# Optimization experiments

Hardware: AMD Instinct MI355X
Metric: run time of the kernel (lower is better)

## Reference

```python
import jax, jax.numpy as jnp
import numpy as np

N_NODES = 100000
N_EDGES = 1600000
HIDDEN = 64
N_MID = 3  # num_layers=5 -> 1 first + 3 middle + 1 last


def setup_inputs() -> dict:
    key = jax.random.key(0)
    ks = jax.random.split(key, 12)
    x = jax.random.normal(ks[0], (N_NODES, 1), dtype=jnp.float32)
    edge_index = jax.random.randint(ks[1], (2, N_EDGES), 0, N_NODES, dtype=jnp.int32)
    edge_weight = jax.random.uniform(ks[2], (N_EDGES,), dtype=jnp.float32)
    s0 = 1.0  # fan_in=1
    sh = 1.0 / np.sqrt(HIDDEN)
    Wrel0 = jax.random.normal(ks[3], (HIDDEN, 1), dtype=jnp.float32) * s0
    brel0 = jax.random.normal(ks[4], (HIDDEN,), dtype=jnp.float32) * s0
    Wroot0 = jax.random.normal(ks[5], (HIDDEN, 1), dtype=jnp.float32) * s0
    Wrel_mid = jax.random.normal(ks[6], (N_MID, HIDDEN, HIDDEN), dtype=jnp.float32) * sh
    brel_mid = jax.random.normal(ks[7], (N_MID, HIDDEN), dtype=jnp.float32) * sh
    Wroot_mid = jax.random.normal(ks[8], (N_MID, HIDDEN, HIDDEN), dtype=jnp.float32) * sh
    WrelL = jax.random.normal(ks[9], (1, HIDDEN), dtype=jnp.float32) * sh
    brelL = jax.random.normal(ks[10], (1,), dtype=jnp.float32) * sh
    WrootL = jax.random.normal(ks[11], (1, HIDDEN), dtype=jnp.float32) * sh
    return {"x": x, "edge_index": edge_index, "edge_weight": edge_weight,
            "Wrel0": Wrel0, "brel0": brel0, "Wroot0": Wroot0,
            "Wrel_mid": Wrel_mid, "brel_mid": brel_mid, "Wroot_mid": Wroot_mid,
            "WrelL": WrelL, "brelL": brelL, "WrootL": WrootL}


def reference(x, edge_index, edge_weight, Wrel0, brel0, Wroot0,
              Wrel_mid, brel_mid, Wroot_mid, WrelL, brelL, WrootL):
    src = edge_index[0]
    dst = edge_index[1]
    n = x.shape[0]

    def conv(h, Wrel, brel, Wroot):
        # PyG GraphConv(aggr='add'): lin_rel(sum_j w_ij * h_j) + lin_root(h_i)
        msg = h[src] * edge_weight[:, None]          # [E, C]
        agg = jax.ops.segment_sum(msg, dst, num_segments=n)  # [N, C]
        return agg @ Wrel.T + brel + h @ Wroot.T

    # dropout omitted (deterministic reference); relu after all but last layer
    h = jax.nn.relu(conv(x, Wrel0, brel0, Wroot0))
    for i in range(Wrel_mid.shape[0]):
        h = jax.nn.relu(conv(h, Wrel_mid[i], brel_mid[i], Wroot_mid[i]))
    return conv(h, WrelL, brelL, WrootL)  # [N, 1]
```

## Files before the change

kernel.cpp:

```cpp
#include <hip/hip_runtime.h>
#include <stdint.h>


#define NN 100000
#define NE 1600000
#define HID 64
#define NBKT 391
#define CAP 8192
#define PMAX (NBKT * CAP)
#define TILE 4096
#define EPT 16
#define NTILE ((NE + TILE - 1) / TILE)

typedef __attribute__((ext_vector_type(8))) short bf16x8;
typedef __attribute__((ext_vector_type(4))) float f32x4;
typedef __attribute__((ext_vector_type(2))) unsigned int u32x2;
typedef __attribute__((ext_vector_type(4))) unsigned int u32x4;

__device__ __forceinline__ uint32_t rne_bf16(float v) {
    uint32_t u = __float_as_uint(v);
    return (u + 0x7fffu + ((u >> 16) & 1u)) >> 16;
}


__global__ __launch_bounds__(256) void k_bpart(const int* __restrict__ src,
                                               const int* __restrict__ dst,
                                               const float* __restrict__ w,
                                               int* __restrict__ bcur,
                                               int2* __restrict__ bpairs) {
    __shared__ int  hcnt[NBKT];
    __shared__ int  hoff[NBKT];
    __shared__ int  hadj[NBKT];
    __shared__ int  sc0[512];
    __shared__ int  sc1[512];
    __shared__ int2 sT[TILE];
    __shared__ int  sAdj[TILE];
    int tile0 = blockIdx.x * TILE;
    int t = threadIdx.x;
    for (int i = t; i < NBKT; i += 256) hcnt[i] = 0;
    __syncthreads();

    int   pk[EPT];
    int   bk[EPT];
    float wv[EPT];
    #pragma unroll
    for (int k = 0; k < EPT; k++) {
        int e = tile0 + t + k * 256;
        if (e < NE) {
            int d = dst[e];
            int b = d >> 8;
            pk[k] = (src[e] << 8) | (d & 255);
            wv[k] = w[e];
            bk[k] = b;
            atomicAdd(&hcnt[b], 1);
        } else {
            bk[k] = -1;
        }
    }
    __syncthreads();

    sc0[t]       = (t < NBKT) ? hcnt[t] : 0;
    sc0[t + 256] = (t + 256 < NBKT) ? hcnt[t + 256] : 0;
    __syncthreads();
    int* cur = sc0;
    int* oth = sc1;
    for (int off = 1; off < 512; off <<= 1) {
        int v0 = cur[t]       + ((t       >= off) ? cur[t - off]       : 0);
        int v1 = cur[t + 256] + ((t + 256 >= off) ? cur[t + 256 - off] : 0);
        oth[t] = v0;
        oth[t + 256] = v1;
        __syncthreads();
        int* tmp = cur; cur = oth; oth = tmp;
    }
    for (int i = t; i < NBKT; i += 256) {
        int c = hcnt[i];
        int excl = cur[i] - c;
        hoff[i] = excl;
        int gbase = c ? atomicAdd(&bcur[i], c) : 0;
        hadj[i] = gbase - excl;
        hcnt[i] = 0;
    }
    __syncthreads();

    #pragma unroll
    for (int k = 0; k < EPT; k++) {
        if (bk[k] >= 0) {
            int b = bk[k];
            int pos = hoff[b] + atomicAdd(&hcnt[b], 1);
            sT[pos] = make_int2(pk[k], __float_as_int(wv[k]));
            sAdj[pos] = hadj[b];
        }
    }
    __syncthreads();

    int n = NE - tile0; if (n > TILE) n = TILE;
    for (int j = t; j < n; j += 256)
        bpairs[sAdj[j] + j] = sT[j];
}

__global__ __launch_bounds__(256) void k_bcsr(const int* __restrict__ bcur,
                                              const int2* __restrict__ bpairs,
                                              int* __restrict__ offs,
                                              int* __restrict__ ends,
                                              uint32_t* __restrict__ pairs) {
    __shared__ int2 sE[CAP];
    __shared__ int cnt[256];
    __shared__ int scn[256];
    __shared__ int cur[256];
    int k = blockIdx.x, t = threadIdx.x;
    int base = k * CAP;
    int scnt = bcur[k] - base;
    cnt[t] = 0;
    __syncthreads();
    for (int j = t; j < scnt; j += 256) {
        int2 q = bpairs[base + j];
        sE[j] = q;
        atomicAdd(&cnt[q.x & 255], 1);
    }
    __syncthreads();
    int v = cnt[t], acc = v;
    scn[t] = v;
    __syncthreads();
    for (int off = 1; off < 256; off <<= 1) {
        int u = (t >= off) ? scn[t - off] : 0;
        __syncthreads();
        acc += u;
        scn[t] = acc;
        __syncthreads();
    }
    int excl = acc - v;
    cur[t] = excl;
    int d = (k << 8) + t;
    if (d < NN) {
        offs[d] = base + excl;
        ends[d] = base + excl + v;
    }
    __syncthreads();
    for (int j = t; j < scnt; j += 256) {
        int2 q = sE[j];
        int pos = base + atomicAdd(&cur[q.x & 255], 1);
        uint32_t wb = rne_bf16(__int_as_float(q.y)) & 0x7fffu;
        pairs[pos] = (wb << 17) | (uint32_t)(q.x >> 8);
    }
}


__global__ __launch_bounds__(256) void k_wsplit(const float* __restrict__ Wrel_mid,
                                                const float* __restrict__ Wroot_mid,
                                                uint16_t* __restrict__ WgH,
                                                uint16_t* __restrict__ WgL,
                                                uint16_t* __restrict__ WrH,
                                                uint16_t* __restrict__ WrL,
                                                int* __restrict__ bcur) {
    int i = blockIdx.x * blockDim.x + threadIdx.x;
    if (i < NBKT) bcur[i] = i * CAP;
    if (i >= 3 * 4096) return;
    float a = Wrel_mid[i];
    uint32_t ah = rne_bf16(a);
    float al = a - __uint_as_float(ah << 16);
    WgH[i] = (uint16_t)ah;
    WgL[i] = (uint16_t)rne_bf16(al);
    float b = Wroot_mid[i];
    uint32_t bh = rne_bf16(b);
    float bl = b - __uint_as_float(bh << 16);
    WrH[i] = (uint16_t)bh;
    WrL[i] = (uint16_t)rne_bf16(bl);
}


__device__ __forceinline__ void mfma_epilogue(
        int lane, int w, const uint32_t* sH,
        const uint16_t* __restrict__ WgH, const uint16_t* __restrict__ WgL,
        const uint16_t* __restrict__ WrH, const uint16_t* __restrict__ WrL,
        const float* __restrict__ brel,
        uint16_t* sG, uint16_t* sR) {
    int row = lane & 15;
    int quad = lane >> 4;
    int kb = quad * 8;
    bf16x8 ah0 = *(const bf16x8*)&sH[row * 36 + quad * 4];
    bf16x8 ah1 = *(const bf16x8*)&sH[row * 36 + 16 + quad * 4];
    int oc = w * 16 + row;
    {
        bf16x8 bh0 = *(const bf16x8*)&WgH[oc * 64 + kb];
        bf16x8 bh1 = *(const bf16x8*)&WgH[oc * 64 + 32 + kb];
        bf16x8 bl0 = *(const bf16x8*)&WgL[oc * 64 + kb];
        bf16x8 bl1 = *(const bf16x8*)&WgL[oc * 64 + 32 + kb];
        f32x4 acc = {0.f, 0.f, 0.f, 0.f};
        acc = __builtin_amdgcn_mfma_f32_16x16x32_bf16(ah0, bh0, acc, 0, 0, 0);
        acc = __builtin_amdgcn_mfma_f32_16x16x32_bf16(ah1, bh1, acc, 0, 0, 0);
        acc = __builtin_amdgcn_mfma_f32_16x16x32_bf16(ah0, bl0, acc, 0, 0, 0);
        acc = __builtin_amdgcn_mfma_f32_16x16x32_bf16(ah1, bl1, acc, 0, 0, 0);
        #pragma unroll
        for (int r = 0; r < 4; r++)
            sG[(quad * 4 + r) * 68 + oc] = (uint16_t)rne_bf16(acc[r]);
    }
    {
        bf16x8 bh0 = *(const bf16x8*)&WrH[oc * 64 + kb];
        bf16x8 bh1 = *(const bf16x8*)&WrH[oc * 64 + 32 + kb];
        bf16x8 bl0 = *(const bf16x8*)&WrL[oc * 64 + kb];
        bf16x8 bl1 = *(const bf16x8*)&WrL[oc * 64 + 32 + kb];
        float bias = brel[oc];
        f32x4 acc = {bias, bias, bias, bias};
        acc = __builtin_amdgcn_mfma_f32_16x16x32_bf16(ah0, bh0, acc, 0, 0, 0);
        acc = __builtin_amdgcn_mfma_f32_16x16x32_bf16(ah1, bh1, acc, 0, 0, 0);
        acc = __builtin_amdgcn_mfma_f32_16x16x32_bf16(ah0, bl0, acc, 0, 0, 0);
        acc = __builtin_amdgcn_mfma_f32_16x16x32_bf16(ah1, bl1, acc, 0, 0, 0);
        #pragma unroll
        for (int r = 0; r < 4; r++)
            sR[(quad * 4 + r) * 68 + oc] = (uint16_t)rne_bf16(acc[r]);
    }
}

__device__ __forceinline__ void epilogue_writeout(
        int tid, int blk16, const uint16_t* sG, const uint16_t* sR,
        uint16_t* __restrict__ Gout, uint16_t* __restrict__ Rout) {
    const uint32_t* sGd = (const uint32_t*)sG;
    const uint32_t* sRd = (const uint32_t*)sR;
    uint32_t* Gd = (uint32_t*)Gout;
    uint32_t* Rd = (uint32_t*)Rout;
    #pragma unroll
    for (int it = 0; it < 2; it++) {
        int idx = it * 256 + tid;
        int nd = idx >> 5, col = idx & 31;
        Gd[(blk16 + nd) * 32 + col] = sGd[nd * 34 + col];
        Rd[(blk16 + nd) * 32 + col] = sRd[nd * 34 + col];
    }
}


__global__ __launch_bounds__(256) void k_l0pre(
        const int* __restrict__ offs, const int* __restrict__ ends,
        const uint32_t* __restrict__ pairs, const float* __restrict__ x,
        const float* __restrict__ Wrel0, const float* __restrict__ brel0,
        const float* __restrict__ Wroot0,
        const uint16_t* __restrict__ WgH, const uint16_t* __restrict__ WgL,
        const uint16_t* __restrict__ WrH, const uint16_t* __restrict__ WrL,
        const float* __restrict__ brel,
        uint16_t* __restrict__ Gout, uint16_t* __restrict__ Rout) {
    __shared__ uint32_t sH[16 * 36];
    __shared__ uint16_t sG[16 * 68];
    __shared__ uint16_t sR[16 * 68];
    int c = threadIdx.x & 63;
    int w = threadIdx.x >> 6;
    int blk16 = blockIdx.x * 16;
    float agg[4];
    #pragma unroll
    for (int t = 0; t < 4; t++) {
        int node = blk16 + w * 4 + t;
        int b = offs[node], e = ends[node];
        float pp = 0.f;
        for (int j = b + c; j < e; j += 64) {
            uint32_t r = pairs[j];
            pp += __uint_as_float((r >> 17) << 16) * x[r & 0x1ffffu];
        }
        for (int o = 32; o > 0; o >>= 1) pp += __shfl_down(pp, o, 64);
        agg[t] = __shfl(pp, 0, 64);
    }
    float wr = Wrel0[c], br = brel0[c], wo = Wroot0[c];
    #pragma unroll
    for (int t = 0; t < 4; t++) {
        int node = blk16 + w * 4 + t;
        float v = agg[t] * wr + br + x[node] * wo;
        v = v > 0.f ? v : 0.f;
        uint32_t hb = rne_bf16(v);
        uint32_t pn = (uint32_t)__shfl_xor((int)hb, 1, 64);
        if (!(c & 1)) sH[(w * 4 + t) * 36 + (c >> 1)] = hb | (pn << 16);
    }
    __syncthreads();
    mfma_epilogue(c, w, sH, WgH, WgL, WrH, WrL, brel, sG, sR);
    __syncthreads();
    epilogue_writeout((int)threadIdx.x, blk16, sG, sR, Gout, Rout);
}

#define TRRA(dst, off) \
    asm volatile("ds_read_b64_tr_b16 %0, %1 offset:" #off \
                 : "=v"(dst) : "v"(trbA))
#define TRRB(dst, off) \
    asm volatile("ds_read_b64_tr_b16 %0, %1 offset:" #off \
                 : "=v"(dst) : "v"(trbB))

template <bool LAST>
__global__ __launch_bounds__(256, 4) void k_aggfused(
        const int* __restrict__ offs, const int* __restrict__ ends,
        const uint32_t* __restrict__ pairs,
        const uint16_t* __restrict__ Gb, const uint16_t* __restrict__ Rb,
        const uint16_t* __restrict__ WgH, const uint16_t* __restrict__ WgL,
        const uint16_t* __restrict__ WrH, const uint16_t* __restrict__ WrL,
        const float* __restrict__ brel,
        uint16_t* __restrict__ Gout, uint16_t* __restrict__ Rout,
        const float* __restrict__ WrelL, const float* __restrict__ WrootL,
        float* __restrict__ sarr, float* __restrict__ rarr) {
    __shared__ uint32_t sH[16 * 36];
    __shared__ __align__(128) char smem[32768];
    int c = threadIdx.x & 63;
    int w = threadIdx.x >> 6;
    int blk16 = blockIdx.x * 16;
    int n0 = blk16 + w * 4;
    int ov = 0;
    if (c < 4) ov = offs[n0 + c];
    else if (c == 4) ov = ends[n0 + 3];
    int bnd[5];
    bnd[0] = __builtin_amdgcn_readlane(ov, 0);
    bnd[1] = __builtin_amdgcn_readlane(ov, 1);
    bnd[2] = __builtin_amdgcn_readlane(ov, 2);
    bnd[3] = __builtin_amdgcn_readlane(ov, 3);
    bnd[4] = __builtin_amdgcn_readlane(ov, 4);

    int arow  = c & 15;
    int kq    = (c >> 4) * 8;
    int eprm  = ((c >> 5) << 2) | ((c >> 1) & 3);
    int lbyte = ((c >> 3) & 3) * 32 + (c & 1) * 16;
    char* stg = smem + w * 8192;
    uint32_t stgOff = (uint32_t)(uintptr_t)
        (__attribute__((address_space(3))) char*)stg;
    uint32_t trbA = stgOff + ((uint32_t)(c >> 4) << 10)
                          + ((uint32_t)(c & 15) << 3);
    uint32_t trbB = trbA + 4096;

    int blo = bnd[0], bhi = bnd[1];
    if (arow == 1) { blo = bnd[1]; bhi = bnd[2]; }
    if (arow == 2) { blo = bnd[2]; bhi = bnd[3]; }
    if (arow == 3) { blo = bnd[3]; bhi = bnd[4]; }
    if (arow >= 4) { blo = 0;      bhi = 0;      }
    uint32_t wid = (uint32_t)(bhi - blo);

    f32x4 acc16[4];
    {
        int ur[4];
        #pragma unroll
        for (int t = 0; t < 4; t++) ur[t] = (int)(uint32_t)Rb[(n0 + t) * 64 + c];
        #pragma unroll
        for (int nb = 0; nb < 4; nb++) {
            int idx = (nb * 16 + (c & 15)) * 4;
            f32x4 ci;
            #pragma unroll
            for (int t = 0; t < 4; t++) {
                uint32_t rv = (uint32_t)__builtin_amdgcn_ds_bpermute(idx, ur[t]);
                ci[t] = __uint_as_float(rv << 16);
            }
            acc16[nb] = ci;
        }
    }

    const char* gbase = (const char*)Gb;
    int j0 = bnd[0] + c; if (j0 > PMAX - 1) j0 = PMAX - 1;
    uint32_t praw = pairs[j0];
    uint32_t p = (bnd[0] + c < bnd[4]) ? praw : 0;

    for (int cb = bnd[0]; cb < bnd[4]; cb += 64) {
        int jn = cb + 64 + c; if (jn > PMAX - 1) jn = PMAX - 1;
        uint32_t pr2 = pairs[jn];
        #pragma unroll
        for (int i = 0; i < 4; i++) {
            uint32_t r = (uint32_t)__builtin_amdgcn_ds_bpermute(
                (eprm + i * 8) * 4, (int)p);
            uint32_t voff = ((r & 0x1ffffu) << 7) + (uint32_t)lbyte;
            __builtin_amdgcn_global_load_lds(
                (const __attribute__((address_space(1))) void*)(gbase + voff),
                (__attribute__((address_space(3))) void*)(stg + i * 1024),
                16, 0, 0);
        }
        #pragma unroll
        for (int i = 0; i < 4; i++) {
            uint32_t r = (uint32_t)__builtin_amdgcn_ds_bpermute(
                (32 + eprm + i * 8) * 4, (int)p);
            uint32_t voff = ((r & 0x1ffffu) << 7) + (uint32_t)lbyte;
            __builtin_amdgcn_global_load_lds(
                (const __attribute__((address_space(1))) void*)(gbase + voff),
                (__attribute__((address_space(3))) void*)(stg + 4096 + i * 1024),
                16, 0, 0);
        }
        uint32_t mA[8], mB[8];
        int dbA = cb + kq - blo;
        int dbB = cb + 32 + kq - blo;
        #pragma unroll
        for (int q = 0; q < 8; q++) {
            uint32_t rq = (uint32_t)__builtin_amdgcn_ds_bpermute(
                (kq + q) * 4, (int)p);
            mA[q] = ((uint32_t)(dbA + q) < wid) ? (rq >> 17) : 0u;
        }
        #pragma unroll
        for (int q = 0; q < 8; q++) {
            uint32_t rq = (uint32_t)__builtin_amdgcn_ds_bpermute(
                (32 + kq + q) * 4, (int)p);
            mB[q] = ((uint32_t)(dbB + q) < wid) ? (rq >> 17) : 0u;
        }
        u32x4 aav = { mA[0] | (mA[1] << 16), mA[2] | (mA[3] << 16),
                      mA[4] | (mA[5] << 16), mA[6] | (mA[7] << 16) };
        u32x4 abv = { mB[0] | (mB[1] << 16), mB[2] | (mB[3] << 16),
                      mB[4] | (mB[5] << 16), mB[6] | (mB[7] << 16) };
        bf16x8 afA = __builtin_bit_cast(bf16x8, aav);
        bf16x8 afB = __builtin_bit_cast(bf16x8, abv);
        asm volatile("s_waitcnt vmcnt(4)" ::: "memory");
        {
            u32x2 tb0, tb1, tb2, tb3, tb4, tb5, tb6, tb7;
            TRRA(tb0, 0);   TRRA(tb1, 512);
            TRRA(tb2, 128); TRRA(tb3, 640);
            TRRA(tb4, 256); TRRA(tb5, 768);
            TRRA(tb6, 384); TRRA(tb7, 896);
            asm volatile("s_waitcnt lgkmcnt(0)" ::: "memory");
            __builtin_amdgcn_sched_barrier(0);
            u32x4 bb0 = { tb0.x, tb0.y, tb1.x, tb1.y };
            acc16[0] = __builtin_amdgcn_mfma_f32_16x16x32_bf16(
                afA, __builtin_bit_cast(bf16x8, bb0), acc16[0], 0, 0, 0);
            u32x4 bb1 = { tb2.x, tb2.y, tb3.x, tb3.y };
            acc16[1] = __builtin_amdgcn_mfma_f32_16x16x32_bf16(
                afA, __builtin_bit_cast(bf16x8, bb1), acc16[1], 0, 0, 0);
            u32x4 bb2 = { tb4.x, tb4.y, tb5.x, tb5.y };
            acc16[2] = __builtin_amdgcn_mfma_f32_16x16x32_bf16(
                afA, __builtin_bit_cast(bf16x8, bb2), acc16[2], 0, 0, 0);
            u32x4 bb3 = { tb6.x, tb6.y, tb7.x, tb7.y };
            acc16[3] = __builtin_amdgcn_mfma_f32_16x16x32_bf16(
                afA, __builtin_bit_cast(bf16x8, bb3), acc16[3], 0, 0, 0);
        }
        asm volatile("s_waitcnt vmcnt(0)" ::: "memory");
        {
            u32x2 tb0, tb1, tb2, tb3, tb4, tb5, tb6, tb7;
            TRRB(tb0, 0);   TRRB(tb1, 512);
            TRRB(tb2, 128); TRRB(tb3, 640);
            TRRB(tb4, 256); TRRB(tb5, 768);
            TRRB(tb6, 384); TRRB(tb7, 896);
            asm volatile("s_waitcnt lgkmcnt(0)" ::: "memory");
            __builtin_amdgcn_sched_barrier(0);
            u32x4 bb0 = { tb0.x, tb0.y, tb1.x, tb1.y };
            acc16[0] = __builtin_amdgcn_mfma_f32_16x16x32_bf16(
                afB, __builtin_bit_cast(bf16x8, bb0), acc16[0], 0, 0, 0);
            u32x4 bb1 = { tb2.x, tb2.y, tb3.x, tb3.y };
            acc16[1] = __builtin_amdgcn_mfma_f32_16x16x32_bf16(
                afB, __builtin_bit_cast(bf16x8, bb1), acc16[1], 0, 0, 0);
            u32x4 bb2 = { tb4.x, tb4.y, tb5.x, tb5.y };
            acc16[2] = __builtin_amdgcn_mfma_f32_16x16x32_bf16(
                afB, __builtin_bit_cast(bf16x8, bb2), acc16[2], 0, 0, 0);
            u32x4 bb3 = { tb6.x, tb6.y, tb7.x, tb7.y };
            acc16[3] = __builtin_amdgcn_mfma_f32_16x16x32_bf16(
                afB, __builtin_bit_cast(bf16x8, bb3), acc16[3], 0, 0, 0);
        }
        p = (cb + 64 + c < bnd[4]) ? pr2 : 0;
    }

    if (!LAST) {
        #pragma unroll
        for (int t = 0; t < 4; t++) {
            #pragma unroll
            for (int nb = 0; nb < 4; nb++) {
                float v = acc16[nb][t];
                v = v > 0.f ? v : 0.f;
                uint32_t hb = rne_bf16(v);
                uint32_t pn2 = (uint32_t)__shfl_xor((int)hb, 1, 64);
                if (!(c & 1) && c < 16)
                    sH[(w * 4 + t) * 36 + nb * 8 + (c >> 1)] = hb | (pn2 << 16);
            }
        }
        __syncthreads();
        uint16_t* sG = (uint16_t*)smem;
        uint16_t* sR = (uint16_t*)(smem + 2176);
        mfma_epilogue(c, w, sH, WgH, WgL, WrH, WrL, brel, sG, sR);
        __syncthreads();
        epilogue_writeout((int)threadIdx.x, blk16, sG, sR, Gout, Rout);
    } else {
        float wl[4], wo[4];
        #pragma unroll
        for (int nb = 0; nb < 4; nb++) {
            wl[nb] = WrelL[nb * 16 + (c & 15)];
            wo[nb] = WrootL[nb * 16 + (c & 15)];
        }
        #pragma unroll
        for (int t = 0; t < 4; t++) {
            float pa = 0.f, pr = 0.f;
            #pragma unroll
            for (int nb = 0; nb < 4; nb++) {
                float v = acc16[nb][t];
                v = v > 0.f ? v : 0.f;
                pa += v * wl[nb];
                pr += v * wo[nb];
            }
            #pragma unroll
            for (int o = 8; o > 0; o >>= 1) {
                pa += __shfl_down(pa, o, 64);
                pr += __shfl_down(pr, o, 64);
            }
            if (c == 0) { sarr[n0 + t] = pa; rarr[n0 + t] = pr; }
        }
    }
}

__global__ __launch_bounds__(256) void k_last(
        const int* __restrict__ offs, const int* __restrict__ ends,
        const uint32_t* __restrict__ pairs,
        const float* __restrict__ sarr, const float* __restrict__ rarr,
        const float* __restrict__ brelL, float* __restrict__ out) {
    int c = threadIdx.x & 63;
    int w = threadIdx.x >> 6;
    int blk16 = blockIdx.x * 16;
    float b0 = brelL[0];
    #pragma unroll
    for (int t = 0; t < 4; t++) {
        int node = blk16 + w * 4 + t;
        int b = offs[node], e = ends[node];
        float pp = 0.f;
        for (int j = b + c; j < e; j += 64) {
            uint32_t r = pairs[j];
            pp += __uint_as_float((r >> 17) << 16) * sarr[r & 0x1ffffu];
        }
        #pragma unroll
        for (int o = 32; o > 0; o >>= 1) pp += __shfl_down(pp, o, 64);
        if (c == 0) out[node] = pp + rarr[node] + b0;
    }
}

extern "C" void kernel_launch(void* const* d_in, const int* in_sizes, int n_in,
                              void* d_out, int out_size, void* d_ws, size_t ws_size,
                              hipStream_t stream) {
    const float* x        = (const float*)d_in[0];
    const int*   ei       = (const int*)d_in[1];
    const float* ew       = (const float*)d_in[2];
    const float* Wrel0    = (const float*)d_in[3];
    const float* brel0    = (const float*)d_in[4];
    const float* Wroot0   = (const float*)d_in[5];
    const float* Wrel_mid = (const float*)d_in[6];
    const float* brel_mid = (const float*)d_in[7];
    const float* Wroot_mid= (const float*)d_in[8];
    const float* WrelL    = (const float*)d_in[9];
    const float* brelL    = (const float*)d_in[10];
    const float* WrootL   = (const float*)d_in[11];
    float* out = (float*)d_out;

    const int* src  = ei;
    const int* dstp = ei + NE;

    char* w = (char*)d_ws;
    size_t o = 0;
    auto alloc = [&](size_t b) -> void* {
        void* r = (void*)(w + o);
        o += (b + 255) & ~(size_t)255;
        return r;
    };
    int*      offs  = (int*)alloc((size_t)NN * 4);
    int*      ends  = (int*)alloc((size_t)NN * 4);
    int*      bcur  = (int*)alloc((size_t)NBKT * 4);
    uint16_t* WgH   = (uint16_t*)alloc((size_t)3 * 4096 * 2);
    uint16_t* WgL   = (uint16_t*)alloc((size_t)3 * 4096 * 2);
    uint16_t* WrH   = (uint16_t*)alloc((size_t)3 * 4096 * 2);
    uint16_t* WrL   = (uint16_t*)alloc((size_t)3 * 4096 * 2);
    float*    sarr  = (float*)alloc((size_t)NN * 4);
    float*    rarr  = (float*)alloc((size_t)NN * 4);
    uint32_t* pairs = (uint32_t*)alloc((size_t)NBKT * CAP * 4);
    uint16_t* GbA   = (uint16_t*)alloc((size_t)NN * HID * 2);
    uint16_t* RbA   = (uint16_t*)alloc((size_t)NN * HID * 2);
    uint16_t* GbB   = (uint16_t*)alloc((size_t)NN * HID * 2);
    uint16_t* RbB   = (uint16_t*)alloc((size_t)NN * HID * 2);
    (void)RbB;
    int2*  bpairs = (int2*)GbB;

    k_wsplit<<<(3 * 4096 + 255) / 256, 256, 0, stream>>>(
        Wrel_mid, Wroot_mid, WgH, WgL, WrH, WrL, bcur);

    k_bpart<<<NTILE, 256, 0, stream>>>(src, dstp, ew, bcur, bpairs);
    k_bcsr<<<NBKT, 256, 0, stream>>>(bcur, bpairs, offs, ends, pairs);

    k_l0pre<<<NN / 16, 256, 0, stream>>>(
        offs, ends, pairs, x, Wrel0, brel0, Wroot0,
        WgH, WgL, WrH, WrL, brel_mid, GbA, RbA);

    k_aggfused<false><<<NN / 16, 256, 0, stream>>>(
        offs, ends, pairs, GbA, RbA,
        WgH + 4096, WgL + 4096, WrH + 4096, WrL + 4096, brel_mid + HID,
        GbB, RbB, WrelL, WrootL, sarr, rarr);
    k_aggfused<false><<<NN / 16, 256, 0, stream>>>(
        offs, ends, pairs, GbB, RbB,
        WgH + 2 * 4096, WgL + 2 * 4096, WrH + 2 * 4096, WrL + 2 * 4096,
        brel_mid + 2 * HID, GbA, RbA, WrelL, WrootL, sarr, rarr);
    k_aggfused<true><<<NN / 16, 256, 0, stream>>>(
        offs, ends, pairs, GbA, RbA,
        WgH, WgL, WrH, WrL, brel_mid,
        GbB, RbB, WrelL, WrootL, sarr, rarr);

    k_last<<<NN / 16, 256, 0, stream>>>(offs, ends, pairs, sarr, rarr, brelL, out);
}
```

Measured before the change: 324.4 us.

## Fill all 16 MFMA rows per wave and run the epilogue per wave

Each wave now aggregates 16 destination nodes, one per row of the 16x16 MFMA tile, where before it handled 4 nodes and left 12 rows empty. A block therefore covers 64 nodes and the grid shrinks fourfold. The dense epilogue (Wrel/Wroot MFMAs and writeout) is rewritten to run independently per wave in that wave's staging LDS, with no block-wide __syncthreads, and launch bounds are raised to 5 blocks per SM. The aim is to cut wasted MFMA work and block-level synchronisation, at the cost of longer per-wave edge ranges, more tail imbalance, and possible register pressure.

```diff
diff --git a/kernel.cpp b/kernel.cpp
--- a/kernel.cpp
+++ b/kernel.cpp
@@ -280,7 +280,7 @@
                  : "=v"(dst) : "v"(trbB))
 
 template <bool LAST>
-__global__ __launch_bounds__(256, 4) void k_aggfused(
+__global__ __launch_bounds__(256, 5) void k_aggfused(
         const int* __restrict__ offs, const int* __restrict__ ends,
         const uint32_t* __restrict__ pairs,
         const uint16_t* __restrict__ Gb, const uint16_t* __restrict__ Rb,
@@ -290,24 +290,21 @@
         uint16_t* __restrict__ Gout, uint16_t* __restrict__ Rout,
         const float* __restrict__ WrelL, const float* __restrict__ WrootL,
         float* __restrict__ sarr, float* __restrict__ rarr) {
-    __shared__ uint32_t sH[16 * 36];
     __shared__ __align__(128) char smem[32768];
     int c = threadIdx.x & 63;
     int w = threadIdx.x >> 6;
-    int blk16 = blockIdx.x * 16;
-    int n0 = blk16 + w * 4;
-    int ov = 0;
-    if (c < 4) ov = offs[n0 + c];
-    else if (c == 4) ov = ends[n0 + 3];
-    int bnd[5];
-    bnd[0] = __builtin_amdgcn_readlane(ov, 0);
-    bnd[1] = __builtin_amdgcn_readlane(ov, 1);
-    bnd[2] = __builtin_amdgcn_readlane(ov, 2);
-    bnd[3] = __builtin_amdgcn_readlane(ov, 3);
-    bnd[4] = __builtin_amdgcn_readlane(ov, 4);
-
-    int arow  = c & 15;
-    int kq    = (c >> 4) * 8;
+    int n0 = blockIdx.x * 64 + w * 16;
+
+    int myNode = n0 + (c & 15);
+    int nodeOK = myNode < NN;
+    int nclamp = nodeOK ? myNode : NN - 1;
+    int blo = offs[nclamp];
+    int bhi = nodeOK ? ends[nclamp] : blo;
+    uint32_t wid = (uint32_t)(bhi - blo);
+    int start  = __builtin_amdgcn_readlane(blo, 0);
+    int finish = __builtin_amdgcn_readlane(bhi, 15);
+
+    int kq = (c >> 4) * 8;
     int eprm  = ((c >> 5) << 2) | ((c >> 1) & 3);
     int lbyte = ((c >> 3) & 3) * 32 + (c & 1) * 16;
     char* stg = smem + w * 8192;
@@ -317,37 +314,24 @@
                           + ((uint32_t)(c & 15) << 3);
     uint32_t trbB = trbA + 4096;
 
-    int blo = bnd[0], bhi = bnd[1];
-    if (arow == 1) { blo = bnd[1]; bhi = bnd[2]; }
-    if (arow == 2) { blo = bnd[2]; bhi = bnd[3]; }
-    if (arow == 3) { blo = bnd[3]; bhi = bnd[4]; }
-    if (arow >= 4) { blo = 0;      bhi = 0;      }
-    uint32_t wid = (uint32_t)(bhi - blo);
-
     f32x4 acc16[4];
-    {
-        int ur[4];
-        #pragma unroll
-        for (int t = 0; t < 4; t++) ur[t] = (int)(uint32_t)Rb[(n0 + t) * 64 + c];
-        #pragma unroll
-        for (int nb = 0; nb < 4; nb++) {
-            int idx = (nb * 16 + (c & 15)) * 4;
-            f32x4 ci;
-            #pragma unroll
-            for (int t = 0; t < 4; t++) {
-                uint32_t rv = (uint32_t)__builtin_amdgcn_ds_bpermute(idx, ur[t]);
-                ci[t] = __uint_as_float(rv << 16);
-            }
-            acc16[nb] = ci;
+    #pragma unroll
+    for (int nb = 0; nb < 4; nb++) {
+        #pragma unroll
+        for (int t = 0; t < 4; t++) {
+            int node = n0 + (c >> 4) * 4 + t;
+            int ncl = node < NN ? node : NN - 1;
+            uint32_t rv = (uint32_t)Rb[ncl * 64 + nb * 16 + (c & 15)];
+            acc16[nb][t] = __uint_as_float(rv << 16);
         }
     }
 
     const char* gbase = (const char*)Gb;
-    int j0 = bnd[0] + c; if (j0 > PMAX - 1) j0 = PMAX - 1;
+    int j0 = start + c; if (j0 > PMAX - 1) j0 = PMAX - 1;
     uint32_t praw = pairs[j0];
-    uint32_t p = (bnd[0] + c < bnd[4]) ? praw : 0;
-
-    for (int cb = bnd[0]; cb < bnd[4]; cb += 64) {
+    uint32_t p = (start + c < finish) ? praw : 0;
+
+    for (int cb = start; cb < finish; cb += 64) {
         int jn = cb + 64 + c; if (jn > PMAX - 1) jn = PMAX - 1;
         uint32_t pr2 = pairs[jn];
         #pragma unroll
@@ -435,10 +419,11 @@
             acc16[3] = __builtin_amdgcn_mfma_f32_16x16x32_bf16(
                 afB, __builtin_bit_cast(bf16x8, bb3), acc16[3], 0, 0, 0);
         }
-        p = (cb + 64 + c < bnd[4]) ? pr2 : 0;
+        p = (cb + 64 + c < finish) ? pr2 : 0;
     }
 
     if (!LAST) {
+        uint32_t* sHw = (uint32_t*)(smem + w * 8192);
         #pragma unroll
         for (int t = 0; t < 4; t++) {
             #pragma unroll
@@ -447,16 +432,69 @@
                 v = v > 0.f ? v : 0.f;
                 uint32_t hb = rne_bf16(v);
                 uint32_t pn2 = (uint32_t)__shfl_xor((int)hb, 1, 64);
-                if (!(c & 1) && c < 16)
-                    sH[(w * 4 + t) * 36 + nb * 8 + (c >> 1)] = hb | (pn2 << 16);
+                if (!(c & 1))
+                    sHw[((c >> 4) * 4 + t) * 36 + nb * 8 + ((c & 15) >> 1)]
+                        = hb | (pn2 << 16);
             }
         }
-        __syncthreads();
-        uint16_t* sG = (uint16_t*)smem;
-        uint16_t* sR = (uint16_t*)(smem + 2176);
-        mfma_epilogue(c, w, sH, WgH, WgL, WrH, WrL, brel, sG, sR);
-        __syncthreads();
-        epilogue_writeout((int)threadIdx.x, blk16, sG, sR, Gout, Rout);
+        asm volatile("s_waitcnt lgkmcnt(0)" ::: "memory");
+        __builtin_amdgcn_sched_barrier(0);
+        uint16_t* sGw = (uint16_t*)(smem + w * 8192 + 2304);
+        uint16_t* sRw = (uint16_t*)(smem + w * 8192 + 2304 + 2176);
+        int row = c & 15;
+        int quad = c >> 4;
+        int kb = quad * 8;
+        bf16x8 ah0 = *(const bf16x8*)&sHw[row * 36 + quad * 4];
+        bf16x8 ah1 = *(const bf16x8*)&sHw[row * 36 + 16 + quad * 4];
+        #pragma unroll
+        for (int ob = 0; ob < 4; ob++) {
+            int oc = ob * 16 + row;
+            {
+                bf16x8 bh0 = *(const bf16x8*)&WgH[oc * 64 + kb];
+                bf16x8 bh1 = *(const bf16x8*)&WgH[oc * 64 + 32 + kb];
+                bf16x8 bl0 = *(const bf16x8*)&WgL[oc * 64 + kb];
+                bf16x8 bl1 = *(const bf16x8*)&WgL[oc * 64 + 32 + kb];
+                f32x4 acc = {0.f, 0.f, 0.f, 0.f};
+                acc = __builtin_amdgcn_mfma_f32_16x16x32_bf16(ah0, bh0, acc, 0, 0, 0);
+                acc = __builtin_amdgcn_mfma_f32_16x16x32_bf16(ah1, bh1, acc, 0, 0, 0);
+                acc = __builtin_amdgcn_mfma_f32_16x16x32_bf16(ah0, bl0, acc, 0, 0, 0);
+                acc = __builtin_amdgcn_mfma_f32_16x16x32_bf16(ah1, bl1, acc, 0, 0, 0);
+                #pragma unroll
+                for (int r = 0; r < 4; r++)
+                    sGw[(quad * 4 + r) * 68 + oc] = (uint16_t)rne_bf16(acc[r]);
+            }
+            {
+                bf16x8 bh0 = *(const bf16x8*)&WrH[oc * 64 + kb];
+                bf16x8 bh1 = *(const bf16x8*)&WrH[oc * 64 + 32 + kb];
+                bf16x8 bl0 = *(const bf16x8*)&WrL[oc * 64 + kb];
+                bf16x8 bl1 = *(const bf16x8*)&WrL[oc * 64 + 32 + kb];
+                float bias = brel[oc];
+                f32x4 acc = {bias, bias, bias, bias};
+                acc = __builtin_amdgcn_mfma_f32_16x16x32_bf16(ah0, bh0, acc, 0, 0, 0);
+                acc = __builtin_amdgcn_mfma_f32_16x16x32_bf16(ah1, bh1, acc, 0, 0, 0);
+                acc = __builtin_amdgcn_mfma_f32_16x16x32_bf16(ah0, bl0, acc, 0, 0, 0);
+                acc = __builtin_amdgcn_mfma_f32_16x16x32_bf16(ah1, bl1, acc, 0, 0, 0);
+                #pragma unroll
+                for (int r = 0; r < 4; r++)
+                    sRw[(quad * 4 + r) * 68 + oc] = (uint16_t)rne_bf16(acc[r]);
+            }
+        }
+        asm volatile("s_waitcnt lgkmcnt(0)" ::: "memory");
+        __builtin_amdgcn_sched_barrier(0);
+        const uint32_t* sGd = (const uint32_t*)sGw;
+        const uint32_t* sRd = (const uint32_t*)sRw;
+        uint32_t* Gd = (uint32_t*)Gout;
+        uint32_t* Rd = (uint32_t*)Rout;
+        #pragma unroll
+        for (int it = 0; it < 8; it++) {
+            int idx = it * 64 + c;
+            int nd = idx >> 5, col = idx & 31;
+            int node = n0 + nd;
+            if (node < NN) {
+                Gd[node * 32 + col] = sGd[nd * 34 + col];
+                Rd[node * 32 + col] = sRd[nd * 34 + col];
+            }
+        }
     } else {
         float wl[4], wo[4];
         #pragma unroll
@@ -479,7 +517,8 @@
                 pa += __shfl_down(pa, o, 64);
                 pr += __shfl_down(pr, o, 64);
             }
-            if (c == 0) { sarr[n0 + t] = pa; rarr[n0 + t] = pr; }
+            int node = n0 + (c >> 4) * 4 + t;
+            if (!(c & 15) && node < NN) { sarr[node] = pa; rarr[node] = pr; }
         }
     }
 }
@@ -562,15 +601,16 @@
         offs, ends, pairs, x, Wrel0, brel0, Wroot0,
         WgH, WgL, WrH, WrL, brel_mid, GbA, RbA);
 
-    k_aggfused<false><<<NN / 16, 256, 0, stream>>>(
+    int nagg = (NN + 63) / 64;
+    k_aggfused<false><<<nagg, 256, 0, stream>>>(
         offs, ends, pairs, GbA, RbA,
         WgH + 4096, WgL + 4096, WrH + 4096, WrL + 4096, brel_mid + HID,
         GbB, RbB, WrelL, WrootL, sarr, rarr);
-    k_aggfused<false><<<NN / 16, 256, 0, stream>>>(
+    k_aggfused<false><<<nagg, 256, 0, stream>>>(
         offs, ends, pairs, GbB, RbB,
         WgH + 2 * 4096, WgL + 2 * 4096, WrH + 2 * 4096, WrL + 2 * 4096,
         brel_mid + 2 * HID, GbA, RbA, WrelL, WrootL, sarr, rarr);
-    k_aggfused<true><<<NN / 16, 256, 0, stream>>>(
+    k_aggfused<true><<<nagg, 256, 0, stream>>>(
         offs, ends, pairs, GbA, RbA,
         WgH, WgL, WrH, WrL, brel_mid,
         GbB, RbB, WrelL, WrootL, sarr, rarr);
```

Result: faster. 306.6 us (-5.5%).
